# Performance work log

Hardware: AMD Instinct MI355X
Metric: run time of the kernel (lower is better)

The kernel has to match this reference:

```python
import jax, jax.numpy as jnp
import numpy as np

B = 2048   # batch of molecular configurations
P = 22     # particles (alanine dipeptide)
D = 3      # spatial dims
H = 64     # hidden_nf
L = 5      # n_layers


def _base_edges():
    # fully-connected graph, both directions, same ordering as _create_edges
    r, c = [], []
    for i in range(P):
        for j in range(i + 1, P):
            r += [i, j]
            c += [j, i]
    return np.asarray(r, np.int64), np.asarray(c, np.int64)


def _h_initial():
    at = np.arange(P)
    at[[1, 2, 3]] = 2
    at[[19, 20, 21]] = 20
    at[[11, 12, 13]] = 12
    return jnp.asarray(np.eye(P, dtype=np.float32)[at])  # [P, 22] one-hot


def setup_inputs() -> dict:
    key = jax.random.key(0)
    ks = jax.random.split(key, 17)
    nrm = lambda k, s, sc=0.1: (jax.random.normal(k, s, jnp.float32) * sc)
    br, bc = _base_edges()
    off = np.arange(B)[:, None] * P
    rows = jnp.asarray((br[None, :] + off).ravel(), jnp.int32)  # [B*462]
    cols = jnp.asarray((bc[None, :] + off).ravel(), jnp.int32)
    E_IN = 2 * H + 1 + 1  # [h_i, h_j, radial, edge_attr]
    return {
        "t": jax.random.uniform(ks[0], (B,), jnp.float32),
        "x": jax.random.normal(ks[1], (B, P * D), jnp.float32),
        "h0": _h_initial(),
        "emb_W": nrm(ks[2], (P + 1, H)), "emb_b": jnp.zeros((H,), jnp.float32),
        "We1": nrm(ks[3], (L, E_IN, H)), "be1": jnp.zeros((L, H), jnp.float32),
        "We2": nrm(ks[4], (L, H, H)), "be2": jnp.zeros((L, H), jnp.float32),
        "Wa": nrm(ks[5], (L, H, 1)), "ba": jnp.zeros((L, 1), jnp.float32),
        "Wc1": nrm(ks[6], (L, H, H)), "bc1": jnp.zeros((L, H), jnp.float32),
        "Wc2": nrm(ks[7], (L, H, 1), 0.01),
        "Wn1": nrm(ks[8], (L, 2 * H, H)), "bn1": jnp.zeros((L, H), jnp.float32),
        "Wn2": nrm(ks[9], (L, H, H)), "bn2": jnp.zeros((L, H), jnp.float32),
        "rows": rows, "cols": cols,
    }


def reference(t, x, h0, emb_W, emb_b, We1, be1, We2, be2, Wa, ba,
              Wc1, bc1, Wc2, Wn1, bn1, Wn2, bn2, rows, cols):
    silu = jax.nn.silu
    N = B * P
    x0 = x.reshape(N, D)
    # time appended per node, then embedded to hidden
    h_in = jnp.concatenate([jnp.tile(h0, (B, 1)), jnp.repeat(t, P)[:, None]], axis=1)
    h = h_in @ emb_W + emb_b  # [N, H]
    d0 = x0[rows] - x0[cols]
    edge_attr = jnp.sum(d0 * d0, axis=1, keepdims=True)  # [E, 1] fixed edge feature
    xc = x0
    for l in range(L):
        diff = xc[rows] - xc[cols]                      # [E, 3]
        radial = jnp.sum(diff * diff, axis=1, keepdims=True)
        e = jnp.concatenate([h[rows], h[cols], radial, edge_attr], axis=1)
        m = silu(e @ We1[l] + be1[l])
        m = silu(m @ We2[l] + be2[l])                   # [E, H] edge messages
        m = m * jax.nn.sigmoid(m @ Wa[l] + ba[l])       # attention gate
        phi = silu(m @ Wc1[l] + bc1[l]) @ Wc2[l]        # [E, 1]
        xc = xc + jax.ops.segment_sum(diff * jnp.tanh(phi), rows, num_segments=N)
        agg = jax.ops.segment_sum(m, rows, num_segments=N)  # sum aggregation
        h = h + (silu(jnp.concatenate([h, agg], axis=1) @ Wn1[l] + bn1[l]) @ Wn2[l] + bn2[l])
    vel = (xc - x0).reshape(B, P, D)
    vel = vel - vel.mean(axis=1, keepdims=True)  # remove_mean
    return vel.reshape(B, P * D)
```

## Files before the change

kernel.cpp:

```cpp
#include <hip/hip_runtime.h>

#define PB 22
#define HB 64
#define EB 462
#define NL 5

#define W1T_OFF  0
#define W2T_OFF  40960
#define WC1T_OFF 61440
#define WN1T_OFF 81920
#define WN2T_OFF 122880
#define WTOT     143360

typedef __attribute__((ext_vector_type(8))) short short8v;
typedef __attribute__((ext_vector_type(4))) float f32x4;
typedef __attribute__((ext_vector_type(4))) unsigned uint4v;
typedef __attribute__((ext_vector_type(2))) unsigned uint2v;

#define MFMA16(a,b,c) __builtin_amdgcn_mfma_f32_16x16x32_bf16((a),(b),(c),0,0,0)

__device__ __forceinline__ short tobf(float f){
  unsigned u = __float_as_uint(f);
  return (short)((u + 0x7FFFu + ((u>>16)&1u)) >> 16);
}
__device__ __forceinline__ float bf2f(short h){
  return __uint_as_float(((unsigned)(unsigned short)h) << 16);
}
__device__ __forceinline__ void split2(float v, short &hi, short &lo){
  hi = tobf(v);
  lo = tobf(v - bf2f(hi));
}
__device__ __forceinline__ void splitT(float v, short &hi, short &lo){
  unsigned u = __float_as_uint(v);
  hi = (short)(u >> 16);
  float lf = v - __uint_as_float(u & 0xFFFF0000u);
  lo = (short)(__float_as_uint(lf) >> 16);
}
__device__ __forceinline__ float trunc_res(float v){
  return v - __uint_as_float(__float_as_uint(v) & 0xFFFF0000u);
}
__device__ __forceinline__ unsigned pack_hi(float a, float b){
  return __builtin_amdgcn_perm(__float_as_uint(b), __float_as_uint(a), 0x07060302u);
}
__device__ __forceinline__ unsigned rne_pack(float a, float b){
  unsigned ua = __float_as_uint(a);
  unsigned ub = __float_as_uint(b);
  ua = (ua + 0x7FFFu + ((ua>>16)&1u)) >> 16;
  ub = (ub + 0x7FFFu + ((ub>>16)&1u)) & 0xFFFF0000u;
  return ua | ub;
}
__device__ __forceinline__ float siluf(float x){
  return x * __builtin_amdgcn_rcpf(1.f + __expf(-x));
}
__device__ __forceinline__ float sigf(float x){
  return __builtin_amdgcn_rcpf(1.f + __expf(-x));
}
__device__ __forceinline__ float tanhff(float x){
  return fmaf(-2.f, __builtin_amdgcn_rcpf(__expf(2.f*x) + 1.f), 1.f);
}
__device__ __forceinline__ float xorsum_q(float x){
  x += __shfl_xor(x, 16);
  x += __shfl_xor(x, 32);
  return x;
}

__global__ void prep_weights(const float* __restrict__ We1, const float* __restrict__ We2,
                             const float* __restrict__ Wc1, const float* __restrict__ Wn1,
                             const float* __restrict__ Wn2, short* __restrict__ ws){
  int i = blockIdx.x*256 + threadIdx.x;
  if (i >= WTOT) return;
  float v;
  if (i < W2T_OFF){            int l=i>>13, r=i&8191, n=r>>7, k=r&127; v = We1[(l*130+k)*64+n]; }
  else if (i < WC1T_OFF){ int j=i-W2T_OFF;  int l=j>>12, r=j&4095, n=r>>6, k=r&63; v = We2[(l*64+k)*64+n]; }
  else if (i < WN1T_OFF){ int j=i-WC1T_OFF; int l=j>>12, r=j&4095, n=r>>6, k=r&63;
    int kk = (k>>5)*32 + ((k>>2)&1)*16 + ((k>>3)&3)*4 + (k&3);
    v = Wc1[(l*64+kk)*64+n]; }
  else if (i < WN2T_OFF){ int j=i-WN1T_OFF; int l=j>>13, r=j&8191, n=r>>7, k=r&127; v = Wn1[(l*128+k)*64+n]; }
  else {                  int j=i-WN2T_OFF; int l=j>>12, r=j&4095, n=r>>6, k=r&63; v = Wn2[(l*64+k)*64+n]; }
  short hi, lo;
  split2(v, hi, lo);
  ws[i] = hi; ws[WTOT+i] = lo;
}

#define O_Y1   0
#define O_Y2   5984
#define O_SHBH 11968
#define O_SHBL 15136
#define O_WL2  18304
#define O_WC1  27520
#define O_M    36736
#define O_SCAL 45952
#define O_SXC  46976
#define O_SX0  47344
#define O_SDX  47712
#define O_SER  48080
#define O_SEC  48592
#define POOLSZ 49104

__global__ __launch_bounds__(256, 2)
void egnn12(const float* __restrict__ gt,  const float* __restrict__ gx,
            const float* __restrict__ gh0, const float* __restrict__ embW,
            const float* __restrict__ embB,
            const float* __restrict__ We1, const float* __restrict__ be1,
            const float* __restrict__ be2, const float* __restrict__ Wa,
            const float* __restrict__ ba,  const float* __restrict__ bc1,
            const float* __restrict__ Wc2, const float* __restrict__ bn1,
            const float* __restrict__ bn2,
            const int* __restrict__ rows,  const int* __restrict__ cols,
            const short* __restrict__ wbt, float* __restrict__ out)
{
  const int b    = blockIdx.x;
  const int tid  = threadIdx.x;
  const int lane = tid & 63;
  const int wv   = tid >> 6;
  const int c    = lane & 15;
  const int q    = lane >> 4;

  __shared__ __align__(16) char pool[POOLSZ];
  float* Y1s   = (float*)(pool + O_Y1);
  float* Y2s   = (float*)(pool + O_Y2);
  short* SHBH  = (short*)(pool + O_SHBH);
  short* SHBL  = (short*)(pool + O_SHBL);
  short* WL2   = (short*)(pool + O_WL2);
  float* SAF   = (float*)(pool + O_WL2);
  short* WC1H  = (short*)(pool + O_WC1);
  short* Mb    = (short*)(pool + O_M);
  float* SCALf = (float*)(pool + O_SCAL);
  float* sxc4  = (float*)(pool + O_SXC);
  float* sx04  = (float*)(pool + O_SX0);
  float* sdx4  = (float*)(pool + O_SDX);
  unsigned char* SER = (unsigned char*)(pool + O_SER);
  unsigned char* SEC = (unsigned char*)(pool + O_SEC);
  short* UHI = (short*)(pool + O_Y1);
  short* ULO = (short*)(pool + O_Y2);

  const int nA  = tid >> 4;
  const int fqA = tid & 15;
  const int nB  = 16 + (tid >> 4);
  const bool hasB  = (tid < 96);
  const bool hasTD = (tid >= 96 && tid < 162);
  const int tdn = (tid - 96) / 3, tdk = (tid - 96) % 3;

  const float tb = gt[b];

  for (int i = tid; i < 92; i += 256){
    int node = i >> 2, k = i & 3;
    float v = (k < 3 && node < PB) ? gx[b*66 + node*3 + k] : 0.f;
    sx04[i] = v; sxc4[i] = v;
  }
  for (int k = tid; k < 512; k += 256){
    int r = 21, c2 = 21;
    if (k < EB){
      int n = k % 22, s = k / 22;
      int e;
      if (s < n) e = 2*(21*s - (s*(s-1))/2 + (n - s - 1)) + 1;
      else       e = 2*(21*n - (n*(n-1))/2 + (s - n));
      r  = rows[b*EB+e] - b*PB;
      c2 = cols[b*EB+e] - b*PB;
    }
    SER[k] = (unsigned char)r; SEC[k] = (unsigned char)c2;
  }
  for (int i = tid; i < PB*HB; i += 256){
    int n = i >> 6, j = i & 63;
    float acc = embB[j] + tb*embW[PB*HB + j];
    #pragma unroll
    for (int k = 0; k < PB; k++) acc = fmaf(gh0[n*PB+k], embW[k*HB+j], acc);
    short hi, lo; splitT(acc, hi, lo);
    SHBH[n*72+j] = hi; SHBL[n*72+j] = lo;
  }
  __syncthreads();

  #pragma unroll 1
  for (int l = 0; l < NL; l++){
    if (tid < 92) sdx4[tid] = 0.f;
    if (tid < 64){
      SCALf[      tid] = be2[l*64+tid];
      SCALf[ 64 + tid] = bc1[l*64+tid];
      SCALf[128 + tid] = Wa [l*64+tid];
      SCALf[192 + tid] = Wc2[l*64+tid];
    }
    { const short* g2lo = wbt + WTOT + W2T_OFF + l*4096;
      const short* g1hi = wbt + WC1T_OFF + l*4096;
      for (int i = tid; i < 512; i += 256){
        int col = i>>3, kc = i&7;
        *(short8v*)(WL2  + col*72 + kc*8) = *(const short8v*)(g2lo + col*64 + kc*8);
        *(short8v*)(WC1H + col*72 + kc*8) = *(const short8v*)(g1hi + col*64 + kc*8);
      } }
    #pragma unroll 1
    for (int task = wv; task < 16; task += 4){
      const int Yv = task>>3, Mt = (task>>2)&1, nt = task&3;
      const int arow = Mt*16 + c, arowR = arow < PB ? arow : PB-1;
      const short* bp = wbt + W1T_OFF + (l*64 + nt*16 + c)*128 + Yv*64;
      const float initv = Yv ? 0.f : be1[l*64 + nt*16 + c];
      f32x4 acc = {initv, initv, initv, initv};
      #pragma unroll
      for (int kt = 0; kt < 2; kt++){
        short8v ah = *(const short8v*)(SHBH + arowR*72 + kt*32 + q*8);
        short8v al = *(const short8v*)(SHBL + arowR*72 + kt*32 + q*8);
        short8v bh = *(const short8v*)(bp + kt*32 + q*8);
        short8v bl = *(const short8v*)(bp + WTOT + kt*32 + q*8);
        acc = MFMA16(ah, bh, acc);
        acc = MFMA16(al, bh, acc);
        acc = MFMA16(ah, bl, acc);
      }
      float* Yp = Yv ? Y2s : Y1s;
      #pragma unroll
      for (int r = 0; r < 4; r++){
        int row = Mt*16 + q*4 + r;
        if (row < PB) Yp[row*68 + nt*16 + c] = acc[r];
      }
    }
    short8v W2h[2][4];
    #pragma unroll
    for (int nt = 0; nt < 4; nt++)
      #pragma unroll
      for (int kt = 0; kt < 2; kt++)
        W2h[kt][nt] = *(const short8v*)(wbt + W2T_OFF + (l*64+nt*16+c)*64 + kt*32 + q*8);
    f32x4 w8a[2], w8b[2], w9a[2], w9b[2];
    #pragma unroll
    for (int kt = 0; kt < 2; kt++){
      const float* p8 = We1 + (l*130+128)*64 + kt*32 + q*8;
      w8a[kt] = *(const f32x4*)p8;        w8b[kt] = *(const f32x4*)(p8+4);
      w9a[kt] = *(const f32x4*)(p8+64);   w9b[kt] = *(const f32x4*)(p8+68);
    }
    const float bav = ba[l];
    __syncthreads();

    f32x4 gA = {0.f,0.f,0.f,0.f}, gB = {0.f,0.f,0.f,0.f};
    float tdacc = 0.f;
    #pragma unroll 1
    for (int ch = 0; ch < 8; ch++){
      {
        const int e = (ch*4 + wv)*16 + c;
        const int sl = wv*16 + c;
        const int nr = SER[e], nc = SEC[e];
        const f32x4 xr = *(const f32x4*)(sxc4 + nr*4);
        const f32x4 xn = *(const f32x4*)(sxc4 + nc*4);
        const float d0 = xr[0]-xn[0], d1 = xr[1]-xn[1], d2 = xr[2]-xn[2];
        const float rad = d0*d0 + d1*d1 + d2*d2;
        const f32x4 zr = *(const f32x4*)(sx04 + nr*4);
        const f32x4 zn = *(const f32x4*)(sx04 + nc*4);
        const float g0 = zr[0]-zn[0], g1 = zr[1]-zn[1], g2 = zr[2]-zn[2];
        const float ea = g0*g0 + g1*g1 + g2*g2;
        short8v m1h[2], m1l[2];
        #pragma unroll
        for (int kt = 0; kt < 2; kt++){
          const f32x4 ya = *(const f32x4*)(Y1s + nr*68 + kt*32 + q*8);
          const f32x4 yb = *(const f32x4*)(Y1s + nr*68 + kt*32 + q*8 + 4);
          const f32x4 za = *(const f32x4*)(Y2s + nc*68 + kt*32 + q*8);
          const f32x4 zb = *(const f32x4*)(Y2s + nc*68 + kt*32 + q*8 + 4);
          float s0 = siluf(fmaf(rad, w8a[kt][0], fmaf(ea, w9a[kt][0], ya[0]+za[0])));
          float s1 = siluf(fmaf(rad, w8a[kt][1], fmaf(ea, w9a[kt][1], ya[1]+za[1])));
          float s2 = siluf(fmaf(rad, w8a[kt][2], fmaf(ea, w9a[kt][2], ya[2]+za[2])));
          float s3 = siluf(fmaf(rad, w8a[kt][3], fmaf(ea, w9a[kt][3], ya[3]+za[3])));
          float s4 = siluf(fmaf(rad, w8b[kt][0], fmaf(ea, w9b[kt][0], yb[0]+zb[0])));
          float s5 = siluf(fmaf(rad, w8b[kt][1], fmaf(ea, w9b[kt][1], yb[1]+zb[1])));
          float s6 = siluf(fmaf(rad, w8b[kt][2], fmaf(ea, w9b[kt][2], yb[2]+zb[2])));
          float s7 = siluf(fmaf(rad, w8b[kt][3], fmaf(ea, w9b[kt][3], yb[3]+zb[3])));
          uint4v hU, lU;
          hU[0] = pack_hi(s0,s1); hU[1] = pack_hi(s2,s3);
          hU[2] = pack_hi(s4,s5); hU[3] = pack_hi(s6,s7);
          lU[0] = pack_hi(trunc_res(s0),trunc_res(s1)); lU[1] = pack_hi(trunc_res(s2),trunc_res(s3));
          lU[2] = pack_hi(trunc_res(s4),trunc_res(s5)); lU[3] = pack_hi(trunc_res(s6),trunc_res(s7));
          m1h[kt] = __builtin_bit_cast(short8v, hU);
          m1l[kt] = __builtin_bit_cast(short8v, lU);
        }
        f32x4 acc2[4];
        #pragma unroll
        for (int nt = 0; nt < 4; nt++)
          acc2[nt] = *(const f32x4*)(SCALf + nt*16 + q*4);
        #pragma unroll
        for (int kt = 0; kt < 2; kt++)
          #pragma unroll
          for (int nt = 0; nt < 4; nt++){
            short8v w2l = *(const short8v*)(WL2 + (nt*16+c)*72 + kt*32 + q*8);
            acc2[nt] = MFMA16(W2h[kt][nt], m1h[kt], acc2[nt]);
            acc2[nt] = MFMA16(w2l,         m1h[kt], acc2[nt]);
            acc2[nt] = MFMA16(W2h[kt][nt], m1l[kt], acc2[nt]);
          }
        float m2[4][4]; float gp = 0.f;
        #pragma unroll
        for (int nt = 0; nt < 4; nt++){
          const f32x4 waq = *(const f32x4*)(SCALf+128 + nt*16 + q*4);
          #pragma unroll
          for (int r = 0; r < 4; r++){
            float mv = siluf(acc2[nt][r]); m2[nt][r] = mv;
            gp = fmaf(mv, waq[r], gp);
          }
        }
        const float gate = sigf(xorsum_q(gp) + bav);
        #pragma unroll
        for (int nt = 0; nt < 4; nt++)
          #pragma unroll
          for (int r = 0; r < 4; r++) m2[nt][r] *= gate;
        #pragma unroll
        for (int nt = 0; nt < 4; nt++){
          uint2v mp;
          mp.x = rne_pack(m2[nt][0], m2[nt][1]);
          mp.y = rne_pack(m2[nt][2], m2[nt][3]);
          *(uint2v*)(Mb + sl*72 + nt*16 + q*4) = mp;
        }
        short8v mgh[2], mgl[2];
        #pragma unroll
        for (int kt = 0; kt < 2; kt++){
          uint4v hU, lU;
          hU[0] = pack_hi(m2[2*kt][0],   m2[2*kt][1]);
          hU[1] = pack_hi(m2[2*kt][2],   m2[2*kt][3]);
          hU[2] = pack_hi(m2[2*kt+1][0], m2[2*kt+1][1]);
          hU[3] = pack_hi(m2[2*kt+1][2], m2[2*kt+1][3]);
          lU[0] = pack_hi(trunc_res(m2[2*kt][0]),   trunc_res(m2[2*kt][1]));
          lU[1] = pack_hi(trunc_res(m2[2*kt][2]),   trunc_res(m2[2*kt][3]));
          lU[2] = pack_hi(trunc_res(m2[2*kt+1][0]), trunc_res(m2[2*kt+1][1]));
          lU[3] = pack_hi(trunc_res(m2[2*kt+1][2]), trunc_res(m2[2*kt+1][3]));
          mgh[kt] = __builtin_bit_cast(short8v, hU);
          mgl[kt] = __builtin_bit_cast(short8v, lU);
        }
        f32x4 acc3[4];
        #pragma unroll
        for (int nt = 0; nt < 4; nt++)
          acc3[nt] = *(const f32x4*)(SCALf+64 + nt*16 + q*4);
        #pragma unroll
        for (int kt = 0; kt < 2; kt++)
          #pragma unroll
          for (int nt = 0; nt < 4; nt++){
            short8v c1 = *(const short8v*)(WC1H + (nt*16+c)*72 + kt*32 + q*8);
            acc3[nt] = MFMA16(c1, mgh[kt], acc3[nt]);
            acc3[nt] = MFMA16(c1, mgl[kt], acc3[nt]);
          }
        float pp = 0.f;
        #pragma unroll
        for (int nt = 0; nt < 4; nt++){
          const f32x4 wcq = *(const f32x4*)(SCALf+192 + nt*16 + q*4);
          #pragma unroll
          for (int r = 0; r < 4; r++)
            pp = fmaf(siluf(acc3[nt][r]), wcq[r], pp);
        }
        const float th = tanhff(xorsum_q(pp));
        if (q == 0){
          float* tdp = (float*)(Mb + sl*72 + 64);
          tdp[0] = d0*th; tdp[1] = d1*th; tdp[2] = d2*th;
        }
      }
      __syncthreads();
      {
        const int B0 = ch*64;
        {
          int jlo = (B0 - nA + 21) / 22;
          int jhi = (B0 + 63 - nA) / 22; if (jhi > 20) jhi = 20;
          for (int j = jlo; j <= jhi; j++){
            const uint2v u = *(const uint2v*)(Mb + (nA + 22*j - B0)*72 + fqA*4);
            gA[0] += __uint_as_float(u.x << 16);
            gA[1] += __uint_as_float(u.x & 0xFFFF0000u);
            gA[2] += __uint_as_float(u.y << 16);
            gA[3] += __uint_as_float(u.y & 0xFFFF0000u);
          }
        }
        if (hasB){
          int jlo = (B0 - nB + 21) / 22;
          int jhi = (B0 + 63 - nB) / 22; if (jhi > 20) jhi = 20;
          for (int j = jlo; j <= jhi; j++){
            const uint2v u = *(const uint2v*)(Mb + (nB + 22*j - B0)*72 + fqA*4);
            gB[0] += __uint_as_float(u.x << 16);
            gB[1] += __uint_as_float(u.x & 0xFFFF0000u);
            gB[2] += __uint_as_float(u.y << 16);
            gB[3] += __uint_as_float(u.y & 0xFFFF0000u);
          }
        }
        if (hasTD){
          int jlo = (B0 - tdn + 21) / 22;
          int jhi = (B0 + 63 - tdn) / 22; if (jhi > 20) jhi = 20;
          for (int j = jlo; j <= jhi; j++)
            tdacc += ((const float*)(Mb + (tdn + 22*j - B0)*72 + 64))[tdk];
        }
      }
      __syncthreads();
    }
    *(f32x4*)(SAF + nA*68 + fqA*4) = gA;
    if (hasB) *(f32x4*)(SAF + nB*68 + fqA*4) = gB;
    if (hasTD) sdx4[tdn*4 + tdk] = tdacc;
    __syncthreads();

    if (tid < 88) sxc4[tid] += sdx4[tid];
    {
      short8v An1h[4], An1l[4];
      #pragma unroll
      for (int kt = 0; kt < 4; kt++){
        const short* p = wbt + WN1T_OFF + (l*64 + wv*16 + c)*128 + kt*32 + q*8;
        An1h[kt] = *(const short8v*)p;
        An1l[kt] = *(const short8v*)(p + WTOT);
      }
      float bn1v[4];
      #pragma unroll
      for (int r = 0; r < 4; r++) bn1v[r] = bn1[l*64 + wv*16 + q*4 + r];
      #pragma unroll 1
      for (int tt = 0; tt < 2; tt++){
        const int node = tt*16 + c;
        const int nodeR = node < PB ? node : PB-1;
        f32x4 acc; acc[0]=bn1v[0]; acc[1]=bn1v[1]; acc[2]=bn1v[2]; acc[3]=bn1v[3];
        #pragma unroll
        for (int kt = 0; kt < 2; kt++){
          short8v bh = *(const short8v*)(SHBH + nodeR*72 + kt*32 + q*8);
          short8v bl = *(const short8v*)(SHBL + nodeR*72 + kt*32 + q*8);
          acc = MFMA16(An1h[kt], bh, acc);
          acc = MFMA16(An1l[kt], bh, acc);
          acc = MFMA16(An1h[kt], bl, acc);
        }
        #pragma unroll
        for (int kt = 2; kt < 4; kt++){
          const f32x4 fa = *(const f32x4*)(SAF + nodeR*68 + (kt-2)*32 + q*8);
          const f32x4 fb = *(const f32x4*)(SAF + nodeR*68 + (kt-2)*32 + q*8 + 4);
          uint4v hU, lU;
          hU[0] = pack_hi(fa[0],fa[1]); hU[1] = pack_hi(fa[2],fa[3]);
          hU[2] = pack_hi(fb[0],fb[1]); hU[3] = pack_hi(fb[2],fb[3]);
          lU[0] = pack_hi(trunc_res(fa[0]),trunc_res(fa[1])); lU[1] = pack_hi(trunc_res(fa[2]),trunc_res(fa[3]));
          lU[2] = pack_hi(trunc_res(fb[0]),trunc_res(fb[1])); lU[3] = pack_hi(trunc_res(fb[2]),trunc_res(fb[3]));
          short8v bh = __builtin_bit_cast(short8v, hU);
          short8v bl = __builtin_bit_cast(short8v, lU);
          acc = MFMA16(An1h[kt], bh, acc);
          acc = MFMA16(An1l[kt], bh, acc);
          acc = MFMA16(An1h[kt], bl, acc);
        }
        if (node < PB){
          float s0 = siluf(acc[0]), s1 = siluf(acc[1]), s2 = siluf(acc[2]), s3 = siluf(acc[3]);
          uint2v hu, lu;
          hu.x = pack_hi(s0,s1); hu.y = pack_hi(s2,s3);
          lu.x = pack_hi(trunc_res(s0),trunc_res(s1)); lu.y = pack_hi(trunc_res(s2),trunc_res(s3));
          *(uint2v*)(UHI + node*72 + wv*16 + q*4) = hu;
          *(uint2v*)(ULO + node*72 + wv*16 + q*4) = lu;
        }
      }
    }
    __syncthreads();

    {
      short8v An2h[2], An2l[2];
      #pragma unroll
      for (int kt = 0; kt < 2; kt++){
        const short* p = wbt + WN2T_OFF + (l*64 + wv*16 + c)*64 + kt*32 + q*8;
        An2h[kt] = *(const short8v*)p;
        An2l[kt] = *(const short8v*)(p + WTOT);
      }
      float bn2v[4];
      #pragma unroll
      for (int r = 0; r < 4; r++) bn2v[r] = bn2[l*64 + wv*16 + q*4 + r];
      #pragma unroll 1
      for (int tt = 0; tt < 2; tt++){
        const int node = tt*16 + c;
        const int nodeR = node < PB ? node : PB-1;
        f32x4 acc; acc[0]=bn2v[0]; acc[1]=bn2v[1]; acc[2]=bn2v[2]; acc[3]=bn2v[3];
        #pragma unroll
        for (int kt = 0; kt < 2; kt++){
          short8v uh = *(const short8v*)(UHI + nodeR*72 + kt*32 + q*8);
          short8v ul = *(const short8v*)(ULO + nodeR*72 + kt*32 + q*8);
          acc = MFMA16(An2h[kt], uh, acc);
          acc = MFMA16(An2l[kt], uh, acc);
          acc = MFMA16(An2h[kt], ul, acc);
        }
        if (node < PB){
          const int idx = node*72 + wv*16 + q*4;
          uint2v hx = *(const uint2v*)(SHBH + idx);
          uint2v lx = *(const uint2v*)(SHBL + idx);
          float nh0 = __uint_as_float(hx.x << 16) + __uint_as_float(lx.x << 16) + acc[0];
          float nh1 = __uint_as_float(hx.x & 0xFFFF0000u) + __uint_as_float(lx.x & 0xFFFF0000u) + acc[1];
          float nh2 = __uint_as_float(hx.y << 16) + __uint_as_float(lx.y << 16) + acc[2];
          float nh3 = __uint_as_float(hx.y & 0xFFFF0000u) + __uint_as_float(lx.y & 0xFFFF0000u) + acc[3];
          uint2v hn, ln;
          hn.x = pack_hi(nh0,nh1); hn.y = pack_hi(nh2,nh3);
          ln.x = pack_hi(trunc_res(nh0),trunc_res(nh1)); ln.y = pack_hi(trunc_res(nh2),trunc_res(nh3));
          *(uint2v*)(SHBH + idx) = hn;
          *(uint2v*)(SHBL + idx) = ln;
        }
      }
    }
    __syncthreads();
  }

  if (tid < 3){
    float s = 0.f;
    for (int p = 0; p < PB; p++) s += sxc4[p*4+tid] - sx04[p*4+tid];
    sdx4[88+tid] = s * (1.f/PB);
  }
  __syncthreads();
  for (int i = tid; i < 66; i += 256){
    int node = i/3, k = i - node*3;
    out[b*66+i] = sxc4[node*4+k] - sx04[node*4+k] - sdx4[88+k];
  }
}

extern "C" void kernel_launch(void* const* d_in, const int* in_sizes, int n_in,
                              void* d_out, int out_size, void* d_ws, size_t ws_size,
                              hipStream_t stream){
  const float* t    = (const float*)d_in[0];
  const float* x    = (const float*)d_in[1];
  const float* h0   = (const float*)d_in[2];
  const float* embW = (const float*)d_in[3];
  const float* embB = (const float*)d_in[4];
  const float* We1  = (const float*)d_in[5];
  const float* be1  = (const float*)d_in[6];
  const float* We2  = (const float*)d_in[7];
  const float* be2  = (const float*)d_in[8];
  const float* Wa   = (const float*)d_in[9];
  const float* ba   = (const float*)d_in[10];
  const float* Wc1  = (const float*)d_in[11];
  const float* bc1  = (const float*)d_in[12];
  const float* Wc2  = (const float*)d_in[13];
  const float* Wn1  = (const float*)d_in[14];
  const float* bn1  = (const float*)d_in[15];
  const float* Wn2  = (const float*)d_in[16];
  const float* bn2  = (const float*)d_in[17];
  const int* rows   = (const int*)d_in[18];
  const int* cols   = (const int*)d_in[19];
  short* wbt = (short*)d_ws;

  hipLaunchKernelGGL(prep_weights, dim3((WTOT+255)/256), dim3(256), 0, stream,
                     We1, We2, Wc1, Wn1, Wn2, wbt);
  hipLaunchKernelGGL(egnn12, dim3(2048), dim3(256), 0, stream,
                     t, x, h0, embW, embB, We1, be1, be2, Wa, ba, bc1, Wc2,
                     bn1, bn2, rows, cols, (const short*)wbt, (float*)d_out);
}
```

Measured before the change: 650.8 us.

## Double block size to 512 threads, halving edge chunks per workgroup

Raises the workgroup from 4 to 8 waves per graph. The edge loop now runs 4 chunks of 128 edges instead of 8 chunks of 64, and the message buffer in shared memory grows to hold the larger chunk. The node aggregation is redistributed so each thread handles one node row, and each wave takes one 16x16 tile of the node MLP instead of looping over two. The aim is more parallelism and fewer barriers per layer, at the cost of more LDS and register pressure per block, which may lower occupancy.

```diff
diff --git a/kernel.cpp b/kernel.cpp
--- a/kernel.cpp
+++ b/kernel.cpp
@@ -89,16 +89,16 @@
 #define O_WL2  18304
 #define O_WC1  27520
 #define O_M    36736
-#define O_SCAL 45952
-#define O_SXC  46976
-#define O_SX0  47344
-#define O_SDX  47712
-#define O_SER  48080
-#define O_SEC  48592
-#define POOLSZ 49104
-
-__global__ __launch_bounds__(256, 2)
-void egnn12(const float* __restrict__ gt,  const float* __restrict__ gx,
+#define O_SCAL 55168
+#define O_SXC  56192
+#define O_SX0  56560
+#define O_SDX  56928
+#define O_SER  57296
+#define O_SEC  57808
+#define POOLSZ 58320
+
+__global__ __launch_bounds__(512, 2)
+void egnn13(const float* __restrict__ gt,  const float* __restrict__ gx,
             const float* __restrict__ gh0, const float* __restrict__ embW,
             const float* __restrict__ embB,
             const float* __restrict__ We1, const float* __restrict__ be1,
@@ -115,6 +115,8 @@
   const int wv   = tid >> 6;
   const int c    = lane & 15;
   const int q    = lane >> 4;
+  const int Mt   = wv >> 2;
+  const int nb   = wv & 3;
 
   __shared__ __align__(16) char pool[POOLSZ];
   float* Y1s   = (float*)(pool + O_Y1);
@@ -136,19 +138,18 @@
 
   const int nA  = tid >> 4;
   const int fqA = tid & 15;
-  const int nB  = 16 + (tid >> 4);
-  const bool hasB  = (tid < 96);
-  const bool hasTD = (tid >= 96 && tid < 162);
-  const int tdn = (tid - 96) / 3, tdk = (tid - 96) % 3;
+  const bool hasA  = (tid < 352);
+  const bool hasTD = (tid >= 352 && tid < 418);
+  const int tdn = (tid - 352) / 3, tdk = (tid - 352) % 3;
 
   const float tb = gt[b];
 
-  for (int i = tid; i < 92; i += 256){
+  for (int i = tid; i < 92; i += 512){
     int node = i >> 2, k = i & 3;
     float v = (k < 3 && node < PB) ? gx[b*66 + node*3 + k] : 0.f;
     sx04[i] = v; sxc4[i] = v;
   }
-  for (int k = tid; k < 512; k += 256){
+  for (int k = tid; k < 512; k += 512){
     int r = 21, c2 = 21;
     if (k < EB){
       int n = k % 22, s = k / 22;
@@ -160,7 +161,7 @@
     }
     SER[k] = (unsigned char)r; SEC[k] = (unsigned char)c2;
   }
-  for (int i = tid; i < PB*HB; i += 256){
+  for (int i = tid; i < PB*HB; i += 512){
     int n = i >> 6, j = i & 63;
     float acc = embB[j] + tb*embW[PB*HB + j];
     #pragma unroll
@@ -181,15 +182,15 @@
     }
     { const short* g2lo = wbt + WTOT + W2T_OFF + l*4096;
       const short* g1hi = wbt + WC1T_OFF + l*4096;
-      for (int i = tid; i < 512; i += 256){
+      for (int i = tid; i < 512; i += 512){
         int col = i>>3, kc = i&7;
         *(short8v*)(WL2  + col*72 + kc*8) = *(const short8v*)(g2lo + col*64 + kc*8);
         *(short8v*)(WC1H + col*72 + kc*8) = *(const short8v*)(g1hi + col*64 + kc*8);
       } }
     #pragma unroll 1
-    for (int task = wv; task < 16; task += 4){
-      const int Yv = task>>3, Mt = (task>>2)&1, nt = task&3;
-      const int arow = Mt*16 + c, arowR = arow < PB ? arow : PB-1;
+    for (int task = wv; task < 16; task += 8){
+      const int Yv = task>>3, Mtt = (task>>2)&1, nt = task&3;
+      const int arow = Mtt*16 + c, arowR = arow < PB ? arow : PB-1;
       const short* bp = wbt + W1T_OFF + (l*64 + nt*16 + c)*128 + Yv*64;
       const float initv = Yv ? 0.f : be1[l*64 + nt*16 + c];
       f32x4 acc = {initv, initv, initv, initv};
@@ -206,7 +207,7 @@
       float* Yp = Yv ? Y2s : Y1s;
       #pragma unroll
       for (int r = 0; r < 4; r++){
-        int row = Mt*16 + q*4 + r;
+        int row = Mtt*16 + q*4 + r;
         if (row < PB) Yp[row*68 + nt*16 + c] = acc[r];
       }
     }
@@ -226,12 +227,12 @@
     const float bav = ba[l];
     __syncthreads();
 
-    f32x4 gA = {0.f,0.f,0.f,0.f}, gB = {0.f,0.f,0.f,0.f};
+    f32x4 gA = {0.f,0.f,0.f,0.f};
     float tdacc = 0.f;
     #pragma unroll 1
-    for (int ch = 0; ch < 8; ch++){
+    for (int ch = 0; ch < 4; ch++){
       {
-        const int e = (ch*4 + wv)*16 + c;
+        const int e = (ch*8 + wv)*16 + c;
         const int sl = wv*16 + c;
         const int nr = SER[e], nc = SEC[e];
         const f32x4 xr = *(const f32x4*)(sxc4 + nr*4);
@@ -343,10 +344,10 @@
       }
       __syncthreads();
       {
-        const int B0 = ch*64;
-        {
+        const int B0 = ch*128;
+        if (hasA){
           int jlo = (B0 - nA + 21) / 22;
-          int jhi = (B0 + 63 - nA) / 22; if (jhi > 20) jhi = 20;
+          int jhi = (B0 + 127 - nA) / 22; if (jhi > 20) jhi = 20;
           for (int j = jlo; j <= jhi; j++){
             const uint2v u = *(const uint2v*)(Mb + (nA + 22*j - B0)*72 + fqA*4);
             gA[0] += __uint_as_float(u.x << 16);
@@ -355,28 +356,16 @@
             gA[3] += __uint_as_float(u.y & 0xFFFF0000u);
           }
         }
-        if (hasB){
-          int jlo = (B0 - nB + 21) / 22;
-          int jhi = (B0 + 63 - nB) / 22; if (jhi > 20) jhi = 20;
-          for (int j = jlo; j <= jhi; j++){
-            const uint2v u = *(const uint2v*)(Mb + (nB + 22*j - B0)*72 + fqA*4);
-            gB[0] += __uint_as_float(u.x << 16);
-            gB[1] += __uint_as_float(u.x & 0xFFFF0000u);
-            gB[2] += __uint_as_float(u.y << 16);
-            gB[3] += __uint_as_float(u.y & 0xFFFF0000u);
-          }
-        }
         if (hasTD){
           int jlo = (B0 - tdn + 21) / 22;
-          int jhi = (B0 + 63 - tdn) / 22; if (jhi > 20) jhi = 20;
+          int jhi = (B0 + 127 - tdn) / 22; if (jhi > 20) jhi = 20;
           for (int j = jlo; j <= jhi; j++)
             tdacc += ((const float*)(Mb + (tdn + 22*j - B0)*72 + 64))[tdk];
         }
       }
       __syncthreads();
     }
-    *(f32x4*)(SAF + nA*68 + fqA*4) = gA;
-    if (hasB) *(f32x4*)(SAF + nB*68 + fqA*4) = gB;
+    if (hasA) *(f32x4*)(SAF + nA*68 + fqA*4) = gA;
     if (hasTD) sdx4[tdn*4 + tdk] = tdacc;
     __syncthreads();
 
@@ -385,16 +374,15 @@
       short8v An1h[4], An1l[4];
       #pragma unroll
       for (int kt = 0; kt < 4; kt++){
-        const short* p = wbt + WN1T_OFF + (l*64 + wv*16 + c)*128 + kt*32 + q*8;
+        const short* p = wbt + WN1T_OFF + (l*64 + nb*16 + c)*128 + kt*32 + q*8;
         An1h[kt] = *(const short8v*)p;
         An1l[kt] = *(const short8v*)(p + WTOT);
       }
       float bn1v[4];
       #pragma unroll
-      for (int r = 0; r < 4; r++) bn1v[r] = bn1[l*64 + wv*16 + q*4 + r];
-      #pragma unroll 1
-      for (int tt = 0; tt < 2; tt++){
-        const int node = tt*16 + c;
+      for (int r = 0; r < 4; r++) bn1v[r] = bn1[l*64 + nb*16 + q*4 + r];
+      {
+        const int node = Mt*16 + c;
         const int nodeR = node < PB ? node : PB-1;
         f32x4 acc; acc[0]=bn1v[0]; acc[1]=bn1v[1]; acc[2]=bn1v[2]; acc[3]=bn1v[3];
         #pragma unroll
@@ -425,8 +413,8 @@
           uint2v hu, lu;
           hu.x = pack_hi(s0,s1); hu.y = pack_hi(s2,s3);
           lu.x = pack_hi(trunc_res(s0),trunc_res(s1)); lu.y = pack_hi(trunc_res(s2),trunc_res(s3));
-          *(uint2v*)(UHI + node*72 + wv*16 + q*4) = hu;
-          *(uint2v*)(ULO + node*72 + wv*16 + q*4) = lu;
+          *(uint2v*)(UHI + node*72 + nb*16 + q*4) = hu;
+          *(uint2v*)(ULO + node*72 + nb*16 + q*4) = lu;
         }
       }
     }
@@ -436,16 +424,15 @@
       short8v An2h[2], An2l[2];
       #pragma unroll
       for (int kt = 0; kt < 2; kt++){
-        const short* p = wbt + WN2T_OFF + (l*64 + wv*16 + c)*64 + kt*32 + q*8;
+        const short* p = wbt + WN2T_OFF + (l*64 + nb*16 + c)*64 + kt*32 + q*8;
         An2h[kt] = *(const short8v*)p;
         An2l[kt] = *(const short8v*)(p + WTOT);
       }
       float bn2v[4];
       #pragma unroll
-      for (int r = 0; r < 4; r++) bn2v[r] = bn2[l*64 + wv*16 + q*4 + r];
-      #pragma unroll 1
-      for (int tt = 0; tt < 2; tt++){
-        const int node = tt*16 + c;
+      for (int r = 0; r < 4; r++) bn2v[r] = bn2[l*64 + nb*16 + q*4 + r];
+      {
+        const int node = Mt*16 + c;
         const int nodeR = node < PB ? node : PB-1;
         f32x4 acc; acc[0]=bn2v[0]; acc[1]=bn2v[1]; acc[2]=bn2v[2]; acc[3]=bn2v[3];
         #pragma unroll
@@ -457,7 +444,7 @@
           acc = MFMA16(An2h[kt], ul, acc);
         }
         if (node < PB){
-          const int idx = node*72 + wv*16 + q*4;
+          const int idx = node*72 + nb*16 + q*4;
           uint2v hx = *(const uint2v*)(SHBH + idx);
           uint2v lx = *(const uint2v*)(SHBL + idx);
           float nh0 = __uint_as_float(hx.x << 16) + __uint_as_float(lx.x << 16) + acc[0];
@@ -481,7 +468,7 @@
     sdx4[88+tid] = s * (1.f/PB);
   }
   __syncthreads();
-  for (int i = tid; i < 66; i += 256){
+  for (int i = tid; i < 66; i += 512){
     int node = i/3, k = i - node*3;
     out[b*66+i] = sxc4[node*4+k] - sx04[node*4+k] - sdx4[88+k];
   }
@@ -514,7 +501,7 @@
 
   hipLaunchKernelGGL(prep_weights, dim3((WTOT+255)/256), dim3(256), 0, stream,
                      We1, We2, Wc1, Wn1, Wn2, wbt);
-  hipLaunchKernelGGL(egnn12, dim3(2048), dim3(256), 0, stream,
+  hipLaunchKernelGGL(egnn13, dim3(2048), dim3(512), 0, stream,
                      t, x, h0, embW, embB, We1, be1, be2, Wa, ba, bc1, Wc2,
                      bn1, bn2, rows, cols, (const short*)wbt, (float*)d_out);
 }
```

Result: slower. 863.0 us (+32.6%).
